# Performance work log

Measured on AMD Instinct MI355X. Metric: run time of the kernel, lower is better.

Reference implementation:

```python
import jax, jax.numpy as jnp
import numpy as np

HEADS = 8
BUCKETS = 64
TEMP = 0.75
SINKHORN_ITER = 5
EPS = 1e-6


def setup_inputs() -> dict:
    key = jax.random.key(0)
    ks = jax.random.split(key, 6)
    b, t, d = 2, 4096, 1024
    x = jax.random.normal(ks[0], (b, t, d), dtype=jnp.float32)
    gumbel_u = jax.random.uniform(ks[1], (b * HEADS, BUCKETS, BUCKETS), dtype=jnp.float32)
    w_qkv = jax.random.normal(ks[2], (d, 3 * d), dtype=jnp.float32) * (d ** -0.5)
    sort_w = jax.random.normal(ks[3], (1, HEADS, (d // HEADS) * 2, BUCKETS), dtype=jnp.float32)
    w_out = jax.random.normal(ks[4], (d, d), dtype=jnp.float32) * (d ** -0.5)
    b_out = jax.random.normal(ks[5], (d,), dtype=jnp.float32) * 0.01
    return {"x": x, "gumbel_u": gumbel_u, "w_qkv": w_qkv, "sort_w": sort_w,
            "w_out": w_out, "b_out": b_out}


def reference(x, gumbel_u, w_qkv, sort_w, w_out, b_out):
    b, t, d = x.shape
    h, buckets = HEADS, BUCKETS
    d_h = d // h
    bsz = t // buckets
    bh = b * h

    # qkv projection (no bias) and head merge -> (b*h, t, d_h)
    qkv = x @ w_qkv
    q, k, v = jnp.split(qkv, 3, axis=2)
    def merge_heads(u):
        return u.reshape(b, t, h, d_h).transpose(0, 2, 1, 3).reshape(bh, t, d_h)
    q, k, v = merge_heads(q), merge_heads(k), merge_heads(v)

    # bucket -> (bh, buckets, bsz, d_h)
    b_q = q.reshape(bh, buckets, bsz, d_h)
    b_k = k.reshape(bh, buckets, bsz, d_h)
    b_v = v.reshape(bh, buckets, bsz, d_h)

    # SortNet: bucket sums -> leaky_relu(x @ W), W per-head (2*d_h, buckets)
    sx = jnp.concatenate([b_q.sum(axis=2), b_k.sum(axis=2)], axis=-1)  # (bh, buckets, 2*d_h)
    W = jnp.broadcast_to(sort_w, (b, h, 2 * d_h, buckets)).reshape(bh, 2 * d_h, buckets)
    R = jax.nn.leaky_relu(jnp.einsum('bue,bec->buc', sx, W), negative_slope=0.01)

    # gumbel-sinkhorn (log clamped for finiteness; matches torch when R >= 0)
    g = -jnp.log(-jnp.log(gumbel_u + EPS) + EPS)
    r = (jnp.log(jnp.maximum(R + EPS, EPS)) + g) / TEMP
    for _ in range(SINKHORN_ITER):
        r = r - jax.nn.logsumexp(r, axis=2, keepdims=True)
        r = r - jax.nn.logsumexp(r, axis=1, keepdims=True)
    R = jnp.exp(r)

    # zero all but top-1 along last dim
    idx = jnp.argmax(R, axis=2)
    R = jnp.where(jnp.arange(buckets)[None, None, :] == idx[..., None], R, 0.0)

    # soft-permute buckets of k and v, concat with locals -> (bh, buckets, 2*bsz, d_h)
    k_r = jnp.einsum('buv,bvtd->butd', R, b_k)
    v_r = jnp.einsum('buv,bvtd->butd', R, b_v)
    b_k2 = jnp.concatenate([k_r, b_k], axis=2)
    b_v2 = jnp.concatenate([v_r, b_v], axis=2)

    # bucketed attention; NOTE: scale uses full model dim d (as in source)
    dots = jnp.einsum('buie,buje->buij', b_q, b_k2) * (d ** -0.5)
    attn = jax.nn.softmax(dots, axis=-1)
    out = jnp.einsum('buij,buje->buie', attn, b_v2)  # (bh, buckets, bsz, d_h)

    out = out.reshape(b, h, t, d_h).transpose(0, 2, 1, 3).reshape(b, t, d)
    return out @ w_out + b_out
```

## Files before the change

### kernel.cpp

```cpp
#include <hip/hip_runtime.h>
#include <stdint.h>

#define TEMP_ 0.75f
#define EPS_ 1e-6f

typedef __attribute__((ext_vector_type(8))) short bf16x8;
typedef __attribute__((ext_vector_type(4))) float f32x4;

typedef __attribute__((address_space(1))) void gvoid_t;
typedef __attribute__((address_space(3))) void lvoid_t;

__device__ __forceinline__ void async_ld16(const void* g, void* l) {
  __builtin_amdgcn_global_load_lds((gvoid_t*)g, (lvoid_t*)l, 16, 0, 0);
}

__device__ __forceinline__ float b2f(ushort u) {
  return __builtin_bit_cast(float, (uint32_t)u << 16);
}
__device__ __forceinline__ ushort f2b(float f) {
  uint32_t x = __builtin_bit_cast(uint32_t, f);
  x += 0x7fffu + ((x >> 16) & 1u);
  return (ushort)(x >> 16);
}

__device__ __forceinline__ uint32_t lds_u32(const void* p) {
  return (uint32_t)(uintptr_t)(lvoid_t*)p;
}

__device__ __forceinline__ bf16x8 dsr(uint32_t addr) {
  bf16x8 d;
  asm volatile("ds_read_b128 %0, %1" : "=v"(d) : "v"(addr));
  return d;
}

__global__ __launch_bounds__(256) void prep_fused(
    const float* __restrict__ x, ushort* __restrict__ xb, float* __restrict__ xsum2,
    const float* __restrict__ wqkv, ushort* __restrict__ wqkvT,
    const float* __restrict__ wout, ushort* __restrict__ woutT) {
  __shared__ float tile[32][33];
  const int blk = blockIdx.x;
  const int tid = threadIdx.x;
  if (blk < 256) {
    const int bu = blk >> 1, half = blk & 1;
    const int b = bu >> 6, u = bu & 63;
    const int c = tid * 4;
    const float* src = x + ((size_t)(b * 4096 + u * 64 + half * 32)) * 1024 + c;
    ushort* dst = xb + ((size_t)(b * 4096 + u * 64 + half * 32)) * 1024 + c;
    float s0 = 0.f, s1 = 0.f, s2 = 0.f, s3 = 0.f;
    for (int pos = 0; pos < 32; pos++) {
      float4 v = *(const float4*)(src + (size_t)pos * 1024);
      s0 += v.x; s1 += v.y; s2 += v.z; s3 += v.w;
      ushort4 o;
      o.x = f2b(v.x); o.y = f2b(v.y); o.z = f2b(v.z); o.w = f2b(v.w);
      *(ushort4*)(dst + (size_t)pos * 1024) = o;
    }
    float4 sv = {s0, s1, s2, s3};
    *(float4*)&xsum2[(size_t)blk * 1024 + c] = sv;
    return;
  }
  const float* src;
  ushort* dst;
  int R, C, bx, by;
  if (blk < 256 + 3072) {
    int lin = blk - 256;
    src = wqkv; dst = wqkvT; R = 1024; C = 3072;
    bx = (lin % 96) * 32; by = (lin / 96) * 32;
  } else {
    int lin = blk - 3328;
    src = wout; dst = woutT; R = 1024; C = 1024;
    bx = (lin % 32) * 32; by = (lin / 32) * 32;
  }
  int tx = tid & 31, ty = tid >> 5;
  #pragma unroll
  for (int i = 0; i < 32; i += 8)
    tile[ty + i][tx] = src[(size_t)(by + ty + i) * C + bx + tx];
  __syncthreads();
  #pragma unroll
  for (int i = 0; i < 32; i += 8)
    dst[(size_t)(bx + ty + i) * R + by + tx] = f2b(tile[tx][ty + i]);
}

__global__ __launch_bounds__(256) void sx_gemm_partial(
    const float* __restrict__ xsum2, const float* __restrict__ wqkv,
    float* __restrict__ SXP) {
  __shared__ float xs[128 * 36];
  const int cb = blockIdx.x;
  const int rt = blockIdx.y;
  const int kc = blockIdx.z;
  const int tid = threadIdx.x;
  #pragma unroll
  for (int it = 0; it < 16; ++it) {
    int idx = it * 256 + tid;
    int k = idx & 127, r = idx >> 7;
    int bu = rt * 32 + r;
    int kk = kc * 128 + k;
    xs[k * 36 + r] =
        xsum2[(size_t)(bu * 2) * 1024 + kk] + xsum2[(size_t)(bu * 2 + 1) * 1024 + kk];
  }
  __syncthreads();
  const int n = cb * 256 + tid;
  float acc[32];
  #pragma unroll
  for (int r = 0; r < 32; r++) acc[r] = 0.f;
  #pragma unroll 2
  for (int k = 0; k < 128; k++) {
    float w = wqkv[(size_t)(kc * 128 + k) * 3072 + n];
    #pragma unroll
    for (int j = 0; j < 8; ++j) {
      f32x4 a = *(const f32x4*)&xs[k * 36 + j * 4];
      acc[j * 4 + 0] += a[0] * w;
      acc[j * 4 + 1] += a[1] * w;
      acc[j * 4 + 2] += a[2] * w;
      acc[j * 4 + 3] += a[3] * w;
    }
  }
  #pragma unroll
  for (int r = 0; r < 32; r++)
    SXP[(size_t)(kc * 128 + rt * 32 + r) * 2048 + n] = acc[r];
}

__global__ __launch_bounds__(256) void sx_reduce(
    const float* __restrict__ SXP, float* __restrict__ SX) {
  const int bu = blockIdx.y;
  const int n = blockIdx.x * 256 + threadIdx.x;
  float s = 0.f;
  #pragma unroll
  for (int kc = 0; kc < 8; kc++)
    s += SXP[(size_t)(kc * 128 + bu) * 2048 + n];
  const int head = (n >> 7) & 7;
  const int e2 = ((n >> 10) << 7) | (n & 127);
  const int b = bu >> 6, u = bu & 63;
  SX[((size_t)((b * 8 + head) * 256) + e2) * 64 + u] = s;
}

__global__ __launch_bounds__(256) void sortnet_sinkhorn(
    const float* __restrict__ SX, const float* __restrict__ sortw,
    const float* __restrict__ gum, int* __restrict__ idxArr,
    float* __restrict__ wgtArr) {
  __shared__ float sxl[64 * 64];
  __shared__ float wl[64 * 64];
  __shared__ float rr[64 * 65];
  __shared__ float redA[256];
  __shared__ float redB[256];
  __shared__ int redi[256];
  const int bh = blockIdx.x, tid = threadIdx.x, head = bh & 7;
  const int ui = tid & 15, ci = tid >> 4;

  float acc[4][4];
  #pragma unroll
  for (int i = 0; i < 4; i++)
    #pragma unroll
    for (int j = 0; j < 4; j++) acc[i][j] = 0.f;

  const f32x4* SX4 = (const f32x4*)(SX + (size_t)bh * 16384);
  const f32x4* W4 = (const f32x4*)(sortw + (size_t)head * 16384);
  f32x4* sxl4 = (f32x4*)sxl;
  f32x4* wl4 = (f32x4*)wl;

  #pragma unroll 1
  for (int ch = 0; ch < 4; ch++) {
    __syncthreads();
    #pragma unroll 1
    for (int g = tid; g < 1024; g += 256) {
      sxl4[g] = SX4[ch * 1024 + g];
      wl4[g] = W4[ch * 1024 + g];
    }
    __syncthreads();
    #pragma unroll 2
    for (int e = 0; e < 64; e++) {
      f32x4 a = sxl4[e * 16 + ui];
      f32x4 w = wl4[e * 16 + ci];
      #pragma unroll
      for (int i = 0; i < 4; i++)
        #pragma unroll
        for (int j = 0; j < 4; j++) acc[i][j] += a[i] * w[j];
    }
  }

  #pragma unroll
  for (int i = 0; i < 4; i++)
    #pragma unroll
    for (int j = 0; j < 4; j++) {
      int u = ui * 4 + i, c = ci * 4 + j;
      float dot = acc[i][j];
      float r0 = dot > 0.f ? dot : 0.01f * dot;
      float gu = gum[(size_t)bh * 4096 + u * 64 + c];
      float inner = -logf(gu + EPS_) + EPS_;
      float g = -logf(fmaxf(inner, 1e-38f));
      rr[u * 65 + c] = (logf(fmaxf(r0 + EPS_, EPS_)) + g) / TEMP_;
    }
  __syncthreads();

  const int su = tid & 63, sq = tid >> 6;
  #pragma unroll 1
  for (int it = 0; it < 5; it++) {
    {
      float pm = -1e30f;
      #pragma unroll
      for (int j = 0; j < 16; j++) pm = fmaxf(pm, rr[su * 65 + sq * 16 + j]);
      redA[sq * 64 + su] = pm;
      __syncthreads();
      float m = fmaxf(fmaxf(redA[su], redA[64 + su]), fmaxf(redA[128 + su], redA[192 + su]));
      float ps = 0.f;
      #pragma unroll
      for (int j = 0; j < 16; j++) ps += expf(rr[su * 65 + sq * 16 + j] - m);
      redB[sq * 64 + su] = ps;
      __syncthreads();
      float l = m + logf(redB[su] + redB[64 + su] + redB[128 + su] + redB[192 + su]);
      #pragma unroll
      for (int j = 0; j < 16; j++) rr[su * 65 + sq * 16 + j] -= l;
      __syncthreads();
    }
    {
      float pm = -1e30f;
      #pragma unroll
      for (int j = 0; j < 16; j++) pm = fmaxf(pm, rr[(sq * 16 + j) * 65 + su]);
      redA[sq * 64 + su] = pm;
      __syncthreads();
      float m = fmaxf(fmaxf(redA[su], redA[64 + su]), fmaxf(redA[128 + su], redA[192 + su]));
      float ps = 0.f;
      #pragma unroll
      for (int j = 0; j < 16; j++) ps += expf(rr[(sq * 16 + j) * 65 + su] - m);
      redB[sq * 64 + su] = ps;
      __syncthreads();
      float l = m + logf(redB[su] + redB[64 + su] + redB[128 + su] + redB[192 + su]);
      #pragma unroll
      for (int j = 0; j < 16; j++) rr[(sq * 16 + j) * 65 + su] -= l;
      __syncthreads();
    }
  }

  {
    float pv = -1e30f;
    int pi = 0;
    #pragma unroll
    for (int j = 0; j < 16; j++) {
      float v = rr[su * 65 + sq * 16 + j];
      if (v > pv) { pv = v; pi = sq * 16 + j; }
    }
    redA[sq * 64 + su] = pv;
    redi[sq * 64 + su] = pi;
    __syncthreads();
    if (tid < 64) {
      float best = -1e30f;
      int bi = 0;
      #pragma unroll
      for (int q = 0; q < 4; q++) {
        float v = redA[q * 64 + tid];
        if (v > best) { best = v; bi = redi[q * 64 + tid]; }
      }
      idxArr[bh * 64 + tid] = bi;
      wgtArr[bh * 64 + tid] = expf(fminf(best, 80.f));
    }
  }
}

__global__ __launch_bounds__(256, 2) void gemm_bt(
    const ushort* __restrict__ A, const ushort* __restrict__ BT,
    int M, int N, int K, int mode,
    const float* __restrict__ bias, float* __restrict__ Cout,
    ushort* __restrict__ Qb, ushort* __restrict__ Kb, ushort* __restrict__ VT) {
  __shared__ ushort As[2][128 * 64];
  __shared__ ushort Bs[2][128 * 64];
  const int tid = threadIdx.x;
  const int wave = tid >> 6, lane = tid & 63;
  const int quad = lane >> 4, l16 = lane & 15;
  const int gx = gridDim.x;
  const int lin = blockIdx.y * gx + blockIdx.x;
  const int nwg = gx * gridDim.y;
  const int swz = (lin & 7) * (nwg >> 3) + (lin >> 3);
  const int bx = swz % gx, by = swz / gx;
  const int m0 = by * 128, n0 = bx * 128;
  const int wm = (wave >> 1) * 64, wn = (wave & 1) * 64;
  const ushort* Ap = A + (uint64_t)m0 * K;
  const ushort* Bp = BT + (uint64_t)n0 * K;

  auto stage = [&](const ushort* G, int k0, ushort* buf) {
    #pragma unroll
    for (int q = 0; q < 4; ++q) {
      int p = q * 256 + tid;
      int row = p >> 3, pp = p & 7;
      int cc = pp ^ (row & 7);
      async_ld16(G + (uint64_t)row * K + k0 + cc * 8,
                 buf + (q * 256 + wave * 64) * 8);
    }
  };

  const uint32_t asB = lds_u32(&As[0][0]);
  const uint32_t bsB = lds_u32(&Bs[0][0]);
  uint32_t aoff[2][4], boff[2][4];
  #pragma unroll
  for (int kk = 0; kk < 2; ++kk) {
    int pc = (kk * 4 + quad) ^ (l16 & 7);
    #pragma unroll
    for (int mt = 0; mt < 4; ++mt) {
      aoff[kk][mt] = (uint32_t)((wm + mt * 16 + l16) * 128 + pc * 16);
      boff[kk][mt] = (uint32_t)((wn + mt * 16 + l16) * 128 + pc * 16);
    }
  }

  f32x4 acc[4][4];
  #pragma unroll
  for (int i = 0; i < 4; i++)
    #pragma unroll
    for (int j = 0; j < 4; j++) acc[i][j] = (f32x4){0.f, 0.f, 0.f, 0.f};

  const int NT = K >> 6;
  stage(Ap, 0, As[0]);
  stage(Bp, 0, Bs[0]);
  stage(Ap, 64, As[1]);
  stage(Bp, 64, Bs[1]);

  #pragma unroll 1
  for (int t = 0; t < NT; ++t) {
    if (t < NT - 1)
      asm volatile("s_waitcnt vmcnt(8)\n\ts_barrier" ::: "memory");
    else
      asm volatile("s_waitcnt vmcnt(0)\n\ts_barrier" ::: "memory");

    const uint32_t ab = asB + (uint32_t)(t & 1) * 16384u;
    const uint32_t bb = bsB + (uint32_t)(t & 1) * 16384u;
    bf16x8 a[2][4], b[2][4];
    #pragma unroll
    for (int kk = 0; kk < 2; ++kk) {
      #pragma unroll
      for (int mt = 0; mt < 4; ++mt) a[kk][mt] = dsr(ab + aoff[kk][mt]);
      #pragma unroll
      for (int nt = 0; nt < 4; ++nt) b[kk][nt] = dsr(bb + boff[kk][nt]);
    }
    asm volatile("s_waitcnt lgkmcnt(8)" ::: "memory");
    __builtin_amdgcn_sched_barrier(0);
    __builtin_amdgcn_s_setprio(1);
    #pragma unroll
    for (int mt = 0; mt < 4; ++mt)
      #pragma unroll
      for (int nt = 0; nt < 4; ++nt)
        acc[mt][nt] = __builtin_amdgcn_mfma_f32_16x16x32_bf16(a[0][mt], b[0][nt], acc[mt][nt], 0, 0, 0);
    __builtin_amdgcn_s_setprio(0);
    asm volatile("s_waitcnt lgkmcnt(0)" ::: "memory");
    __builtin_amdgcn_sched_barrier(0);
    __builtin_amdgcn_s_setprio(1);
    #pragma unroll
    for (int mt = 0; mt < 4; ++mt)
      #pragma unroll
      for (int nt = 0; nt < 4; ++nt)
        acc[mt][nt] = __builtin_amdgcn_mfma_f32_16x16x32_bf16(a[1][mt], b[1][nt], acc[mt][nt], 0, 0, 0);
    __builtin_amdgcn_s_setprio(0);
    asm volatile("s_barrier" ::: "memory");
    if (t + 2 < NT) {
      stage(Ap, (t + 2) * 64, As[t & 1]);
      stage(Bp, (t + 2) * 64, Bs[t & 1]);
    }
  }

  if (mode == 0) {
    #pragma unroll
    for (int mt = 0; mt < 4; mt++) {
      int row = m0 + wm + mt * 16 + quad * 4;
      #pragma unroll
      for (int nt = 0; nt < 4; nt++) {
        int col = n0 + wn + nt * 16 + l16;
        float bv = bias[col];
        #pragma unroll
        for (int r = 0; r < 4; r++)
          Cout[(uint64_t)(row + r) * N + col] = acc[mt][nt][r] + bv;
      }
    }
  } else {
    int which = bx >> 3;
    int head = bx & 7;
    #pragma unroll
    for (int mt = 0; mt < 4; mt++) {
      int mrow = m0 + wm + mt * 16 + quad * 4;
      int bidx = mrow >> 12;
      int ttok = mrow & 4095;
      int u = ttok >> 6, pos = ttok & 63;
      int bh = bidx * 8 + head;
      #pragma unroll
      for (int nt = 0; nt < 4; nt++) {
        int e = wn + nt * 16 + l16;
        if (which == 2) {
          ushort4 pk;
          pk.x = f2b(acc[mt][nt][0]);
          pk.y = f2b(acc[mt][nt][1]);
          pk.z = f2b(acc[mt][nt][2]);
          pk.w = f2b(acc[mt][nt][3]);
          *(ushort4*)&VT[((uint64_t)(bh * 64 + u) * 128 + e) * 64 + pos] = pk;
        } else {
          ushort* dst = (which == 0) ? Qb : Kb;
          #pragma unroll
          for (int r = 0; r < 4; r++)
            dst[((uint64_t)(bh * 64 + u) * 64 + pos + r) * 128 + e] = f2b(acc[mt][nt][r]);
        }
      }
    }
  }
}

#define KSTR 136
__global__ __launch_bounds__(256) void attn_kernel(
    const ushort* __restrict__ Qb, const ushort* __restrict__ Kb,
    const ushort* __restrict__ VT, const int* __restrict__ idxArr,
    const float* __restrict__ wgtArr, ushort* __restrict__ attn_out) {
  __shared__ ushort Qs[64 * KSTR];
  __shared__ ushort Ks[128 * KSTR];
  const int blk = blockIdx.x;
  const int u = blk & 63, bh = blk >> 6;
  const int tid = threadIdx.x, wave = tid >> 6, lane = tid & 63;
  const int quad = lane >> 4, l16 = lane & 15;
  const int vu = idxArr[bh * 64 + u] & 63;
  const float w = wgtArr[bh * 64 + u];

  const ushort* Qsrc = Qb + (uint64_t)(bh * 64 + u) * 8192;
  const ushort* Ksrc0 = Kb + (uint64_t)(bh * 64 + vu) * 8192;
  const ushort* Ksrc1 = Kb + (uint64_t)(bh * 64 + u) * 8192;
  const ushort* Vsrc0 = VT + (uint64_t)(bh * 64 + vu) * 8192;
  const ushort* Vsrc1 = VT + (uint64_t)(bh * 64 + u) * 8192;

  for (int g = tid; g < 64 * 16; g += 256) {
    int eb = g & 15, p = g >> 4;
    *(bf16x8*)&Qs[p * KSTR + eb * 8] = *(const bf16x8*)&Qsrc[p * 128 + eb * 8];
  }
  for (int g = tid; g < 128 * 16; g += 256) {
    int eb = g & 15, j = g >> 4;
    const ushort* s = (j < 64) ? &Ksrc0[j * 128 + eb * 8] : &Ksrc1[(j - 64) * 128 + eb * 8];
    *(bf16x8*)&Ks[j * KSTR + eb * 8] = *(const bf16x8*)s;
  }
  __syncthreads();

  f32x4 S[8];
  #pragma unroll
  for (int nt = 0; nt < 8; nt++) S[nt] = (f32x4){0.f, 0.f, 0.f, 0.f};
  #pragma unroll
  for (int kk = 0; kk < 4; kk++) {
    bf16x8 aq = *(const bf16x8*)&Qs[(wave * 16 + l16) * KSTR + kk * 32 + quad * 8];
    #pragma unroll
    for (int nt = 0; nt < 8; nt++) {
      bf16x8 bk = *(const bf16x8*)&Ks[(nt * 16 + l16) * KSTR + kk * 32 + quad * 8];
      S[nt] = __builtin_amdgcn_mfma_f32_16x16x32_bf16(aq, bk, S[nt], 0, 0, 0);
    }
  }
  __syncthreads();

  for (int g = tid; g < 128 * 16; g += 256) {
    int jb = g & 15, e = g >> 4;
    const ushort* s = (jb < 8) ? &Vsrc0[e * 64 + jb * 8] : &Vsrc1[e * 64 + (jb - 8) * 8];
    *(bf16x8*)&Ks[e * KSTR + jb * 8] = *(const bf16x8*)s;
  }

  const float scale = 0.03125f;
  float rowmax[4] = {-1e30f, -1e30f, -1e30f, -1e30f};
  #pragma unroll
  for (int nt = 0; nt < 8; nt++) {
    float cs = scale * ((nt < 4) ? w : 1.0f);
    #pragma unroll
    for (int r = 0; r < 4; r++) {
      S[nt][r] *= cs;
      rowmax[r] = fmaxf(rowmax[r], S[nt][r]);
    }
  }
  #pragma unroll
  for (int off = 1; off < 16; off <<= 1)
    #pragma unroll
    for (int r = 0; r < 4; r++)
      rowmax[r] = fmaxf(rowmax[r], __shfl_xor(rowmax[r], off, 64));
  float rowsum[4] = {0.f, 0.f, 0.f, 0.f};
  #pragma unroll
  for (int nt = 0; nt < 8; nt++)
    #pragma unroll
    for (int r = 0; r < 4; r++) {
      float p = expf(S[nt][r] - rowmax[r]);
      S[nt][r] = p;
      rowsum[r] += p;
    }
  #pragma unroll
  for (int off = 1; off < 16; off <<= 1)
    #pragma unroll
    for (int r = 0; r < 4; r++)
      rowsum[r] += __shfl_xor(rowsum[r], off, 64);
  float rinv[4];
  #pragma unroll
  for (int r = 0; r < 4; r++) rinv[r] = 1.0f / rowsum[r];

  #pragma unroll
  for (int nt = 0; nt < 8; nt++)
    #pragma unroll
    for (int r = 0; r < 4; r++) {
      float pv = S[nt][r] * rinv[r] * ((nt < 4) ? w : 1.0f);
      Qs[(wave * 16 + quad * 4 + r) * KSTR + nt * 16 + l16] = f2b(pv);
    }
  __syncthreads();

  f32x4 O[8];
  #pragma unroll
  for (int nt = 0; nt < 8; nt++) O[nt] = (f32x4){0.f, 0.f, 0.f, 0.f};
  #pragma unroll
  for (int kk = 0; kk < 4; kk++) {
    bf16x8 ap = *(const bf16x8*)&Qs[(wave * 16 + l16) * KSTR + kk * 32 + quad * 8];
    #pragma unroll
    for (int nt = 0; nt < 8; nt++) {
      bf16x8 bv = *(const bf16x8*)&Ks[(nt * 16 + l16) * KSTR + kk * 32 + quad * 8];
      O[nt] = __builtin_amdgcn_mfma_f32_16x16x32_bf16(ap, bv, O[nt], 0, 0, 0);
    }
  }

  const int bidx = bh >> 3, head = bh & 7;
  uint64_t rowbase =
      (uint64_t)(bidx * 4096 + u * 64 + wave * 16 + quad * 4) * 1024 + head * 128;
  #pragma unroll
  for (int nt = 0; nt < 8; nt++)
    #pragma unroll
    for (int r = 0; r < 4; r++)
      attn_out[rowbase + (uint64_t)r * 1024 + nt * 16 + l16] = f2b(O[nt][r]);
}

extern "C" void kernel_launch(void* const* d_in, const int* in_sizes, int n_in,
                              void* d_out, int out_size, void* d_ws, size_t ws_size,
                              hipStream_t stream) {
  (void)in_sizes; (void)n_in; (void)out_size; (void)ws_size;
  const float* x = (const float*)d_in[0];
  const float* gum = (const float*)d_in[1];
  const float* wqkv = (const float*)d_in[2];
  const float* sortw = (const float*)d_in[3];
  const float* wout = (const float*)d_in[4];
  const float* bout = (const float*)d_in[5];
  float* out = (float*)d_out;

  char* ws = (char*)d_ws;
  size_t off = 0;
  auto alloc = [&](size_t bytes) {
    char* p = ws + off;
    off += (bytes + 255) & ~(size_t)255;
    return p;
  };
  ushort* xb = (ushort*)alloc((size_t)8192 * 1024 * 2);
  float* xsum2 = (float*)alloc((size_t)256 * 1024 * 4);
  ushort* wqkvT = (ushort*)alloc((size_t)3072 * 1024 * 2);
  ushort* woutT = (ushort*)alloc((size_t)1024 * 1024 * 2);
  float* SX = (float*)alloc((size_t)16 * 256 * 64 * 4);
  ushort* Qb = (ushort*)alloc((size_t)16 * 64 * 64 * 128 * 2);
  ushort* Kb = (ushort*)alloc((size_t)16 * 64 * 64 * 128 * 2);
  ushort* VT = (ushort*)alloc((size_t)16 * 64 * 128 * 64 * 2);
  int* idxArr = (int*)alloc((size_t)16 * 64 * 4);
  float* wgtArr = (float*)alloc((size_t)16 * 64 * 4);
  ushort* attn = xb;
  float* SXP = (float*)Qb;

  prep_fused<<<4352, 256, 0, stream>>>(x, xb, xsum2, wqkv, wqkvT, wout, woutT);
  sx_gemm_partial<<<dim3(8, 4, 8), 256, 0, stream>>>(xsum2, wqkv, SXP);
  sx_reduce<<<dim3(8, 128), 256, 0, stream>>>(SXP, SX);
  sortnet_sinkhorn<<<16, 256, 0, stream>>>(SX, sortw, gum, idxArr, wgtArr);
  gemm_bt<<<dim3(3072 / 128, 8192 / 128), 256, 0, stream>>>(
      xb, wqkvT, 8192, 3072, 1024, 1, nullptr, nullptr, Qb, Kb, VT);
  attn_kernel<<<16 * 64, 256, 0, stream>>>(Qb, Kb, VT, idxArr, wgtArr, attn);
  gemm_bt<<<dim3(1024 / 128, 8192 / 128), 256, 0, stream>>>(
      attn, woutT, 8192, 1024, 1024, 0, bout, out, nullptr, nullptr, nullptr);
}
```

Before: 270.7 us.

## Fold SX reduction into sortnet, split GEMM into QKV and simpler output kernels

Removes the sx_reduce kernel: sx_gemm_partial now writes partials transposed with vector stores, and sortnet_sinkhorn sums the eight K-chunk partials while loading its tile. The shared gemm_bt is split into a QKV-specialised kernel with K fixed at compile time and a separate output-projection GEMM. The output GEMM drops double buffering and the block swizzle, using a single-stage async load into split lo/hi LDS halves with a sync before each step. This saves one launch and an intermediate buffer, but the new output GEMM loses load/compute overlap and may run slower.

Result: no change. 272.7 us (+0.7%).

```diff
diff --git a/kernel.cpp b/kernel.cpp
--- a/kernel.cpp
+++ b/kernel.cpp
@@ -114,27 +114,16 @@
       acc[j * 4 + 3] += a[3] * w;
     }
   }
-  #pragma unroll
-  for (int r = 0; r < 32; r++)
-    SXP[(size_t)(kc * 128 + rt * 32 + r) * 2048 + n] = acc[r];
-}
-
-__global__ __launch_bounds__(256) void sx_reduce(
-    const float* __restrict__ SXP, float* __restrict__ SX) {
-  const int bu = blockIdx.y;
-  const int n = blockIdx.x * 256 + threadIdx.x;
-  float s = 0.f;
-  #pragma unroll
-  for (int kc = 0; kc < 8; kc++)
-    s += SXP[(size_t)(kc * 128 + bu) * 2048 + n];
-  const int head = (n >> 7) & 7;
-  const int e2 = ((n >> 10) << 7) | (n & 127);
-  const int b = bu >> 6, u = bu & 63;
-  SX[((size_t)((b * 8 + head) * 256) + e2) * 64 + u] = s;
+  float* dst = SXP + (size_t)n * 1024 + kc * 128 + rt * 32;
+  #pragma unroll
+  for (int j = 0; j < 8; ++j) {
+    f32x4 v = {acc[j * 4], acc[j * 4 + 1], acc[j * 4 + 2], acc[j * 4 + 3]};
+    *(f32x4*)&dst[j * 4] = v;
+  }
 }
 
 __global__ __launch_bounds__(256) void sortnet_sinkhorn(
-    const float* __restrict__ SX, const float* __restrict__ sortw,
+    const float* __restrict__ SXP, const float* __restrict__ sortw,
     const float* __restrict__ gum, int* __restrict__ idxArr,
     float* __restrict__ wgtArr) {
   __shared__ float sxl[64 * 64];
@@ -143,7 +132,7 @@
   __shared__ float redA[256];
   __shared__ float redB[256];
   __shared__ int redi[256];
-  const int bh = blockIdx.x, tid = threadIdx.x, head = bh & 7;
+  const int bh = blockIdx.x, tid = threadIdx.x, head = bh & 7, b = bh >> 3;
   const int ui = tid & 15, ci = tid >> 4;
 
   float acc[4][4];
@@ -152,7 +141,6 @@
     #pragma unroll
     for (int j = 0; j < 4; j++) acc[i][j] = 0.f;
 
-  const f32x4* SX4 = (const f32x4*)(SX + (size_t)bh * 16384);
   const f32x4* W4 = (const f32x4*)(sortw + (size_t)head * 16384);
   f32x4* sxl4 = (f32x4*)sxl;
   f32x4* wl4 = (f32x4*)wl;
@@ -162,7 +150,16 @@
     __syncthreads();
     #pragma unroll 1
     for (int g = tid; g < 1024; g += 256) {
-      sxl4[g] = SX4[ch * 1024 + g];
+      int e = g >> 4, u4 = g & 15;
+      int n = (ch >> 1) * 1024 + head * 128 + (ch & 1) * 64 + e;
+      const float* p = SXP + (size_t)n * 1024 + b * 64 + u4 * 4;
+      f32x4 s = *(const f32x4*)p;
+      #pragma unroll
+      for (int kc = 1; kc < 8; ++kc) {
+        f32x4 v = *(const f32x4*)(p + kc * 128);
+        s[0] += v[0]; s[1] += v[1]; s[2] += v[2]; s[3] += v[3];
+      }
+      sxl4[g] = s;
       wl4[g] = W4[ch * 1024 + g];
     }
     __syncthreads();
@@ -255,11 +252,10 @@
   }
 }
 
-__global__ __launch_bounds__(256, 2) void gemm_bt(
+__global__ __launch_bounds__(256, 2) void gemm_qkv(
     const ushort* __restrict__ A, const ushort* __restrict__ BT,
-    int M, int N, int K, int mode,
-    const float* __restrict__ bias, float* __restrict__ Cout,
     ushort* __restrict__ Qb, ushort* __restrict__ Kb, ushort* __restrict__ VT) {
+  const int K = 1024;
   __shared__ ushort As[2][128 * 64];
   __shared__ ushort Bs[2][128 * 64];
   const int tid = threadIdx.x;
@@ -353,46 +349,103 @@
     }
   }
 
-  if (mode == 0) {
-    #pragma unroll
-    for (int mt = 0; mt < 4; mt++) {
-      int row = m0 + wm + mt * 16 + quad * 4;
-      #pragma unroll
-      for (int nt = 0; nt < 4; nt++) {
-        int col = n0 + wn + nt * 16 + l16;
-        float bv = bias[col];
+  int which = bx >> 3;
+  int head = bx & 7;
+  #pragma unroll
+  for (int mt = 0; mt < 4; mt++) {
+    int mrow = m0 + wm + mt * 16 + quad * 4;
+    int bidx = mrow >> 12;
+    int ttok = mrow & 4095;
+    int u = ttok >> 6, pos = ttok & 63;
+    int bh = bidx * 8 + head;
+    #pragma unroll
+    for (int nt = 0; nt < 4; nt++) {
+      int e = wn + nt * 16 + l16;
+      if (which == 2) {
+        ushort4 pk;
+        pk.x = f2b(acc[mt][nt][0]);
+        pk.y = f2b(acc[mt][nt][1]);
+        pk.z = f2b(acc[mt][nt][2]);
+        pk.w = f2b(acc[mt][nt][3]);
+        *(ushort4*)&VT[((uint64_t)(bh * 64 + u) * 128 + e) * 64 + pos] = pk;
+      } else {
+        ushort* dst = (which == 0) ? Qb : Kb;
         #pragma unroll
         for (int r = 0; r < 4; r++)
-          Cout[(uint64_t)(row + r) * N + col] = acc[mt][nt][r] + bv;
+          dst[((uint64_t)(bh * 64 + u) * 64 + pos + r) * 128 + e] = f2b(acc[mt][nt][r]);
       }
     }
-  } else {
-    int which = bx >> 3;
-    int head = bx & 7;
-    #pragma unroll
-    for (int mt = 0; mt < 4; mt++) {
-      int mrow = m0 + wm + mt * 16 + quad * 4;
-      int bidx = mrow >> 12;
-      int ttok = mrow & 4095;
-      int u = ttok >> 6, pos = ttok & 63;
-      int bh = bidx * 8 + head;
-      #pragma unroll
-      for (int nt = 0; nt < 4; nt++) {
-        int e = wn + nt * 16 + l16;
-        if (which == 2) {
-          ushort4 pk;
-          pk.x = f2b(acc[mt][nt][0]);
-          pk.y = f2b(acc[mt][nt][1]);
-          pk.z = f2b(acc[mt][nt][2]);
-          pk.w = f2b(acc[mt][nt][3]);
-          *(ushort4*)&VT[((uint64_t)(bh * 64 + u) * 128 + e) * 64 + pos] = pk;
-        } else {
-          ushort* dst = (which == 0) ? Qb : Kb;
-          #pragma unroll
-          for (int r = 0; r < 4; r++)
-            dst[((uint64_t)(bh * 64 + u) * 64 + pos + r) * 128 + e] = f2b(acc[mt][nt][r]);
-        }
-      }
+  }
+}
+
+__global__ __launch_bounds__(256, 2) void gemm_out(
+    const ushort* __restrict__ A, const ushort* __restrict__ BT,
+    int M, int N, int K,
+    const float* __restrict__ bias, float* __restrict__ Cout) {
+  __shared__ ushort As_lo[128 * 32];
+  __shared__ ushort As_hi[128 * 32];
+  __shared__ ushort Bs_lo[128 * 32];
+  __shared__ ushort Bs_hi[128 * 32];
+  const int tid = threadIdx.x;
+  const int wave = tid >> 6, lane = tid & 63;
+  const int quad = lane >> 4, l16 = lane & 15;
+  const int m0 = blockIdx.y * 128, n0 = blockIdx.x * 128;
+  const int wm = (wave >> 1) * 64, wn = (wave & 1) * 64;
+
+  f32x4 acc[4][4];
+  #pragma unroll
+  for (int i = 0; i < 4; i++)
+    #pragma unroll
+    for (int j = 0; j < 4; j++) acc[i][j] = (f32x4){0.f, 0.f, 0.f, 0.f};
+
+  const int srow = wave * 32 + (lane >> 2);
+  const int schunk = (lane & 3) * 8;
+
+  for (int k0 = 0; k0 < K; k0 += 64) {
+    __syncthreads();
+    {
+      const ushort* gA0 = A + (uint64_t)(m0 + srow) * K + k0 + schunk;
+      const ushort* gB0 = BT + (uint64_t)(n0 + srow) * K + k0 + schunk;
+      const int lofs = (wave * 32) * 32;
+      async_ld16(gA0, (ushort*)As_lo + lofs);
+      async_ld16(gA0 + (uint64_t)16 * K, (ushort*)As_lo + lofs + 16 * 32);
+      async_ld16(gA0 + 32, (ushort*)As_hi + lofs);
+      async_ld16(gA0 + (uint64_t)16 * K + 32, (ushort*)As_hi + lofs + 16 * 32);
+      async_ld16(gB0, (ushort*)Bs_lo + lofs);
+      async_ld16(gB0 + (uint64_t)16 * K, (ushort*)Bs_lo + lofs + 16 * 32);
+      async_ld16(gB0 + 32, (ushort*)Bs_hi + lofs);
+      async_ld16(gB0 + (uint64_t)16 * K + 32, (ushort*)Bs_hi + lofs + 16 * 32);
+    }
+    __syncthreads();
+    #pragma unroll
+    for (int kk = 0; kk < 2; kk++) {
+      const ushort* Ab = kk ? As_hi : As_lo;
+      const ushort* Bb = kk ? Bs_hi : Bs_lo;
+      bf16x8 af[4], bfr[4];
+      #pragma unroll
+      for (int mt = 0; mt < 4; mt++)
+        af[mt] = *(const bf16x8*)&Ab[(wm + mt * 16 + l16) * 32 + quad * 8];
+      #pragma unroll
+      for (int nt = 0; nt < 4; nt++)
+        bfr[nt] = *(const bf16x8*)&Bb[(wn + nt * 16 + l16) * 32 + quad * 8];
+      #pragma unroll
+      for (int mt = 0; mt < 4; mt++)
+        #pragma unroll
+        for (int nt = 0; nt < 4; nt++)
+          acc[mt][nt] = __builtin_amdgcn_mfma_f32_16x16x32_bf16(af[mt], bfr[nt], acc[mt][nt], 0, 0, 0);
+    }
+  }
+
+  #pragma unroll
+  for (int mt = 0; mt < 4; mt++) {
+    int row = m0 + wm + mt * 16 + quad * 4;
+    #pragma unroll
+    for (int nt = 0; nt < 4; nt++) {
+      int col = n0 + wn + nt * 16 + l16;
+      float bv = bias[col];
+      #pragma unroll
+      for (int r = 0; r < 4; r++)
+        Cout[(uint64_t)(row + r) * N + col] = acc[mt][nt][r] + bv;
     }
   }
 }
@@ -537,7 +590,6 @@
   float* xsum2 = (float*)alloc((size_t)256 * 1024 * 4);
   ushort* wqkvT = (ushort*)alloc((size_t)3072 * 1024 * 2);
   ushort* woutT = (ushort*)alloc((size_t)1024 * 1024 * 2);
-  float* SX = (float*)alloc((size_t)16 * 256 * 64 * 4);
   ushort* Qb = (ushort*)alloc((size_t)16 * 64 * 64 * 128 * 2);
   ushort* Kb = (ushort*)alloc((size_t)16 * 64 * 64 * 128 * 2);
   ushort* VT = (ushort*)alloc((size_t)16 * 64 * 128 * 64 * 2);
@@ -548,11 +600,9 @@
 
   prep_fused<<<4352, 256, 0, stream>>>(x, xb, xsum2, wqkv, wqkvT, wout, woutT);
   sx_gemm_partial<<<dim3(8, 4, 8), 256, 0, stream>>>(xsum2, wqkv, SXP);
-  sx_reduce<<<dim3(8, 128), 256, 0, stream>>>(SXP, SX);
-  sortnet_sinkhorn<<<16, 256, 0, stream>>>(SX, sortw, gum, idxArr, wgtArr);
-  gemm_bt<<<dim3(3072 / 128, 8192 / 128), 256, 0, stream>>>(
-      xb, wqkvT, 8192, 3072, 1024, 1, nullptr, nullptr, Qb, Kb, VT);
+  sortnet_sinkhorn<<<16, 256, 0, stream>>>(SXP, sortw, gum, idxArr, wgtArr);
+  gemm_qkv<<<dim3(3072 / 128, 8192 / 128), 256, 0, stream>>>(xb, wqkvT, Qb, Kb, VT);
   attn_kernel<<<16 * 64, 256, 0, stream>>>(Qb, Kb, VT, idxArr, wgtArr, attn);
-  gemm_bt<<<dim3(1024 / 128, 8192 / 128), 256, 0, stream>>>(
-      attn, woutT, 8192, 1024, 1024, 0, bout, out, nullptr, nullptr, nullptr);
-}
+  gemm_out<<<dim3(1024 / 128, 8192 / 128), 256, 0, stream>>>(
+      attn, woutT, 8192, 1024, 1024, bout, out);
+}
```
